# Kernel tuning notes

Measured on AMD Instinct MI355X. Metric: run time of the kernel, lower is better.

Reference implementation:

```python
import jax, jax.numpy as jnp
import numpy as np

N_NODES = 100000
N_EDGES = 1600000
D_IN = 128
LAYER_SIZES = [128, 128, 64]


def setup_inputs() -> dict:
    key = jax.random.key(0)
    ks = jax.random.split(key, 12)
    x = jax.random.normal(ks[0], (N_NODES, D_IN), dtype=jnp.float32)
    edge_index = jax.random.randint(ks[1], (2, N_EDGES), 0, N_NODES, dtype=jnp.int64)
    edge_weight = jax.random.uniform(ks[2], (N_EDGES,), dtype=jnp.float32)
    inp = {"x": x, "edge_index": edge_index, "edge_weight": edge_weight}
    dims = [D_IN] + LAYER_SIZES
    for i in range(len(LAYER_SIZES)):
        fan_in, fan_out = dims[i], dims[i + 1]
        # glorot-style init like PyG GCNConv
        scale = jnp.sqrt(6.0 / (fan_in + fan_out)).astype(jnp.float32)
        inp[f"W{i}"] = jax.random.uniform(ks[3 + 2 * i], (fan_in, fan_out), dtype=jnp.float32, minval=-scale, maxval=scale)
        inp[f"b{i}"] = jnp.zeros((fan_out,), dtype=jnp.float32)
    return inp


def _gcn_norm(edge_index, edge_weight, num_nodes):
    # PyG gcn_norm with add_self_loops=True (fill value 1.0)
    src, dst = edge_index[0], edge_index[1]
    loop = jnp.arange(num_nodes, dtype=edge_index.dtype)
    src_full = jnp.concatenate([src, loop])
    dst_full = jnp.concatenate([dst, loop])
    w_full = jnp.concatenate([edge_weight, jnp.ones((num_nodes,), dtype=edge_weight.dtype)])
    deg = jax.ops.segment_sum(w_full, dst_full, num_segments=num_nodes)  # [N]
    deg_inv_sqrt = jnp.where(deg > 0, jax.lax.rsqrt(jnp.where(deg > 0, deg, 1.0)), 0.0)
    norm = deg_inv_sqrt[src_full] * w_full * deg_inv_sqrt[dst_full]  # [E+N]
    return src_full, dst_full, norm


def _gcn_conv(x, src, dst, norm, W, b):
    h = x @ W                                  # [N, d_out] dense transform
    msg = h[src] * norm[:, None]               # [E+N, d_out] gather + scale
    out = jax.ops.segment_sum(msg, dst, num_segments=x.shape[0])  # scatter-add
    return out + b


def reference(x, edge_index, edge_weight, W0, b0, W1, b1, W2, b2):
    N = x.shape[0]
    src, dst, norm = _gcn_norm(edge_index, edge_weight, N)
    x = jax.nn.relu(_gcn_conv(x, src, dst, norm, W0, b0))
    x = jax.nn.relu(_gcn_conv(x, src, dst, norm, W1, b1))
    x = _gcn_conv(x, src, dst, norm, W2, b2)  # no ReLU on final layer
    return x
```

## Files before the change

kernel.cpp:

```cpp
#include <hip/hip_runtime.h>
#include <hip/hip_fp16.h>


typedef __attribute__((ext_vector_type(8))) _Float16 f16x8;
typedef __attribute__((ext_vector_type(4))) float f32x4;
typedef unsigned long long u64;

#define WQ_BITS 15
#define WQ_SCALE 32768.0f
#define WQ_MASK 32767u
#define MAXNP 2048

#define RL(v, k) __builtin_amdgcn_readlane((v), (k))

__global__ __launch_bounds__(256) void k_pre(int* tail, int NP,
                                             const float* __restrict__ W0,
                                             const float* __restrict__ W1,
                                             const float* __restrict__ W2,
                                             __half* __restrict__ wt0,
                                             __half* __restrict__ wt1,
                                             __half* __restrict__ wt2) {
    int id = blockIdx.x * 256 + threadIdx.x;
    if (id < NP) tail[id] = 0;
    if (id < 16384) {
        int n = id >> 7, k = id & 127;
        wt0[id] = __float2half(W0[k * 128 + n]);
    } else if (id < 32768) {
        int j = id - 16384, n = j >> 7, k = j & 127;
        wt1[j] = __float2half(W1[k * 128 + n]);
    } else if (id < 40960) {
        int j = id - 32768, n = j >> 7, k = j & 127;
        wt2[j] = __float2half(W2[k * 64 + n]);
    }
}

__global__ __launch_bounds__(256) void k_bin(const int* __restrict__ src,
                                             const int* __restrict__ dst,
                                             const float* __restrict__ w,
                                             int* tail, u64* __restrict__ glist,
                                             int E, int ecap, int NP, int shift) {
    __shared__ unsigned int h[MAXNP];
    __shared__ int base[MAXNP];
    const int nb = gridDim.x;
    const int per = (E + nb - 1) / nb;
    const int e0 = blockIdx.x * per;
    const int e1 = (e0 + per < E) ? e0 + per : E;

    for (int i = threadIdx.x; i < NP; i += 256) h[i] = 0;
    __syncthreads();
    for (int e = e0 + (int)threadIdx.x; e < e1; e += 256) {
        int p = dst[e] >> shift;
        atomicAdd(&h[p], 1u);
    }
    __syncthreads();
    for (int i = threadIdx.x; i < NP; i += 256) {
        unsigned int c = h[i];
        base[i] = c ? atomicAdd(&tail[i], (int)c) : 0;
    }
    __syncthreads();
    for (int e = e0 + (int)threadIdx.x; e < e1; e += 256) {
        int t = dst[e];
        int p = t >> shift;
        int s = __builtin_nontemporal_load(src + e);
        float we = __builtin_nontemporal_load(w + e);
        int wq = (int)(we * WQ_SCALE + 0.5f);
        wq = (wq < (int)WQ_MASK) ? wq : (int)WQ_MASK;
        u64 v = ((u64)(unsigned)t << 32) |
                ((unsigned)s << WQ_BITS) | (unsigned)wq;
        unsigned int idx = atomicSub(&h[p], 1u) - 1u;
        int pos = base[p] + (int)idx;
        if (pos < ecap) glist[(size_t)p * ecap + pos] = v;
    }
}

__global__ __launch_bounds__(256) void k_fill(const int* __restrict__ tail,
                                              const u64* __restrict__ glist,
                                              int ecap, int* __restrict__ cnt,
                                              float* __restrict__ dinv,
                                              unsigned int* __restrict__ EW,
                                              int cap, int N, int shift) {
    __shared__ unsigned int lcnt[MAXNP];
    __shared__ float lws[MAXNP];
    const int p = blockIdx.x;
    const int np = 1 << shift;
    const int t0 = p << shift;
    for (int i = threadIdx.x; i < np; i += 256) { lcnt[i] = 0; lws[i] = 0.f; }
    __syncthreads();
    int n = tail[p];
    if (n > ecap) n = ecap;
    const u64* L = glist + (size_t)p * ecap;
    for (int j = threadIdx.x; j < n; j += 256) {
        u64 v = L[j];
        int t = (int)(v >> 32);
        int loc = t - t0;
        unsigned int k = atomicAdd(&lcnt[loc], 1u);
        if ((int)k < cap) {
            EW[(size_t)t * cap + k] = (unsigned int)v;
            atomicAdd(&lws[loc], (float)((unsigned int)v & WQ_MASK));
        }
    }
    __syncthreads();
    for (int i = threadIdx.x; i < np; i += 256) {
        int t = t0 + i;
        if (t < N) {
            int c = (int)lcnt[i];
            c = (c < cap) ? c : cap;
            cnt[t] = c;
            dinv[t] = 1.0f / sqrtf(1.0f + lws[i] * (1.0f / WQ_SCALE));
        }
    }
}

template <int BN, bool XFP32>
__global__ __launch_bounds__(256, 4) void k_gemm(const void* __restrict__ Xv,
                                                 const __half* __restrict__ Wt,
                                                 const float* __restrict__ dinv,
                                                 __half* __restrict__ H, int N) {
    const int tid = threadIdx.x;
    const int lane = tid & 63;
    const int wv = tid >> 6;
    const int m = lane & 15;
    const int quad = lane >> 4;
    const int rb = blockIdx.x * 64;
    const int row = rb + wv * 16 + m;
    const int rowc = (row < N) ? row : (N - 1);

    f16x8 xf[4];
    if constexpr (XFP32) {
        const float* X = (const float*)Xv;
#pragma unroll
        for (int s = 0; s < 4; s++) {
            const float4* p = (const float4*)(X + (size_t)rowc * 128 + s * 32 + quad * 8);
            float4 u0 = p[0], u1 = p[1];
            f16x8 f;
            f[0] = (_Float16)u0.x; f[1] = (_Float16)u0.y;
            f[2] = (_Float16)u0.z; f[3] = (_Float16)u0.w;
            f[4] = (_Float16)u1.x; f[5] = (_Float16)u1.y;
            f[6] = (_Float16)u1.z; f[7] = (_Float16)u1.w;
            xf[s] = f;
        }
    } else {
        const __half* X = (const __half*)Xv;
#pragma unroll
        for (int s = 0; s < 4; s++)
            xf[s] = *(const f16x8*)(X + (size_t)rowc * 128 + s * 32 + quad * 8);
    }

    constexpr int NT = BN / 16;
    f32x4 acc[NT];
#pragma unroll
    for (int t = 0; t < NT; t++) acc[t] = (f32x4){0.f, 0.f, 0.f, 0.f};

#pragma unroll
    for (int s = 0; s < 4; s++) {
#pragma unroll
        for (int t = 0; t < NT; t++) {
            f16x8 wf = *(const f16x8*)(Wt + (size_t)(t * 16 + m) * 128 + s * 32 + quad * 8);
            acc[t] = __builtin_amdgcn_mfma_f32_16x16x32_f16(wf, xf[s], acc[t], 0, 0, 0);
        }
    }

    if (row < N) {
        float sc = dinv[row];
#pragma unroll
        for (int t = 0; t < NT; t++) {
            __half2 h0 = __floats2half2_rn(sc * acc[t][0], sc * acc[t][1]);
            __half2 h1 = __floats2half2_rn(sc * acc[t][2], sc * acc[t][3]);
            __half2* dstp = (__half2*)(H + (size_t)row * BN + t * 16 + quad * 4);
            dstp[0] = h0;
            dstp[1] = h1;
        }
    }
}

template <int DOUT, bool RELU>
__global__ __launch_bounds__(256) void k_agg(const __half* __restrict__ H,
                                             const unsigned int* __restrict__ EW,
                                             const int* __restrict__ cnt,
                                             const float* __restrict__ dinv,
                                             const float* __restrict__ bias,
                                             void* __restrict__ Outv,
                                             int N, int cap) {
    int node = blockIdx.x * 4 + (threadIdx.x >> 6);
    if (node >= N) return;
    const int lane = threadIdx.x & 63;

    int c = cnt[node];
    c = (c < cap) ? c : cap;

    unsigned int meta = 0;
    if (lane < c) meta = EW[(size_t)node * cap + lane];

    float dt = dinv[node];

    if constexpr (DOUT == 128) {
        const __half2* H2 = reinterpret_cast<const __half2*>(H);
        float2 hs = __half22float2(H2[(size_t)node * 64 + lane]);
        float a0 = hs.x, a1 = hs.y;
        int k = 0;
        for (; k + 8 <= c; k += 8) {
            __half2 hr[8]; float w[8];
#pragma unroll
            for (int u = 0; u < 8; u++) {
                unsigned int mm = RL(meta, k + u);
                w[u] = (float)(mm & WQ_MASK) * (1.0f / WQ_SCALE);
                hr[u] = H2[(size_t)(mm >> WQ_BITS) * 64 + lane];
            }
#pragma unroll
            for (int u = 0; u < 8; u++) {
                float2 hv = __half22float2(hr[u]);
                a0 = fmaf(w[u], hv.x, a0);
                a1 = fmaf(w[u], hv.y, a1);
            }
        }
        for (; k + 4 <= c; k += 4) {
            __half2 hr[4]; float w[4];
#pragma unroll
            for (int u = 0; u < 4; u++) {
                unsigned int mm = RL(meta, k + u);
                w[u] = (float)(mm & WQ_MASK) * (1.0f / WQ_SCALE);
                hr[u] = H2[(size_t)(mm >> WQ_BITS) * 64 + lane];
            }
#pragma unroll
            for (int u = 0; u < 4; u++) {
                float2 hv = __half22float2(hr[u]);
                a0 = fmaf(w[u], hv.x, a0);
                a1 = fmaf(w[u], hv.y, a1);
            }
        }
        for (; k < c; k++) {
            unsigned int mm = RL(meta, k);
            float w = (float)(mm & WQ_MASK) * (1.0f / WQ_SCALE);
            float2 hv = __half22float2(H2[(size_t)(mm >> WQ_BITS) * 64 + lane]);
            a0 = fmaf(w, hv.x, a0);
            a1 = fmaf(w, hv.y, a1);
        }
        float2 b = reinterpret_cast<const float2*>(bias)[lane];
        a0 = fmaf(dt, a0, b.x);
        a1 = fmaf(dt, a1, b.y);
        if (RELU) { a0 = fmaxf(a0, 0.f); a1 = fmaxf(a1, 0.f); }
        reinterpret_cast<__half2*>(Outv)[(size_t)node * 64 + lane] = __floats2half2_rn(a0, a1);
    } else {
        float a = __half2float(H[(size_t)node * 64 + lane]);
        int k = 0;
        for (; k + 8 <= c; k += 8) {
            __half hr[8]; float w[8];
#pragma unroll
            for (int u = 0; u < 8; u++) {
                unsigned int mm = RL(meta, k + u);
                w[u] = (float)(mm & WQ_MASK) * (1.0f / WQ_SCALE);
                hr[u] = H[(size_t)(mm >> WQ_BITS) * 64 + lane];
            }
#pragma unroll
            for (int u = 0; u < 8; u++) a = fmaf(w[u], __half2float(hr[u]), a);
        }
        for (; k < c; k++) {
            unsigned int mm = RL(meta, k);
            float w = (float)(mm & WQ_MASK) * (1.0f / WQ_SCALE);
            a = fmaf(w, __half2float(H[(size_t)(mm >> WQ_BITS) * 64 + lane]), a);
        }
        a = fmaf(dt, a, bias[lane]);
        if (RELU) a = fmaxf(a, 0.f);
        ((float*)Outv)[(size_t)node * 64 + lane] = a;
    }
}

extern "C" void kernel_launch(void* const* d_in, const int* in_sizes, int n_in,
                              void* d_out, int out_size, void* d_ws, size_t ws_size,
                              hipStream_t stream) {
    const int N = in_sizes[0] / 128;
    const int E = in_sizes[2];

    const float* x  = (const float*)d_in[0];
    const int*   ei = (const int*)d_in[1];
    const int*   src = ei;
    const int*   dst = ei + E;
    const float* ew  = (const float*)d_in[2];
    const float* W0 = (const float*)d_in[3];
    const float* b0 = (const float*)d_in[4];
    const float* W1 = (const float*)d_in[5];
    const float* b1 = (const float*)d_in[6];
    const float* W2 = (const float*)d_in[7];
    const float* b2 = (const float*)d_in[8];

    int shift = 6;
    while ((((N - 1) >> shift) + 1) > MAXNP) shift++;
    const int NP = ((N - 1) >> shift) + 1;

    size_t fixed = (((size_t)N * 4 + 255) & ~(size_t)255)
                 + (((size_t)N * 4 + 255) & ~(size_t)255)
                 + 2 * (((size_t)N * 128 * 2 + 255) & ~(size_t)255)
                 + 3 * 33024
                 + (((size_t)NP * 4 + 255) & ~(size_t)255)
                 + 2048;
    int cap = 64;
    if (ws_size > fixed) {
        size_t avail = (ws_size - fixed) / ((size_t)N * 4);
        if (avail < (size_t)cap) cap = (int)avail;
    } else {
        cap = 0;
    }

    char* p = (char*)d_ws;
    auto alloc = [&](size_t bytes) -> void* {
        void* r = (void*)p;
        p += (bytes + 255) & ~(size_t)255;
        return r;
    };
    int*          cnt  = (int*)alloc((size_t)N * 4);
    float*        dinv = (float*)alloc((size_t)N * 4);
    unsigned int* EW   = (unsigned int*)alloc((size_t)N * cap * 4);
    __half*       bufH = (__half*)alloc((size_t)N * 128 * 2);
    __half*       bufA = (__half*)alloc((size_t)N * 128 * 2);
    __half*       wt0  = (__half*)alloc(16384 * 2);
    __half*       wt1  = (__half*)alloc(16384 * 2);
    __half*       wt2  = (__half*)alloc(8192 * 2);
    int*          tail = (int*)alloc((size_t)NP * 4);

    u64* glist = (u64*)bufH;
    int  ecap  = (int)(((size_t)N * 128 * 2) / ((size_t)NP * 8));

    dim3 blk(256);
    int preN = (NP > 40960) ? NP : 40960;
    dim3 gPre((preN + 255) / 256);
    dim3 gBin(256);
    dim3 gFill(NP);
    dim3 gGemm((N + 63) / 64);
    dim3 gWave((N + 3) / 4);

    k_pre<<<gPre, blk, 0, stream>>>(tail, NP, W0, W1, W2, wt0, wt1, wt2);
    k_bin<<<gBin, blk, 0, stream>>>(src, dst, ew, tail, glist, E, ecap, NP, shift);
    k_fill<<<gFill, blk, 0, stream>>>(tail, glist, ecap, cnt, dinv, EW, cap, N, shift);

    k_gemm<128, true><<<gGemm, blk, 0, stream>>>(x, wt0, dinv, bufH, N);
    k_agg<128, true><<<gWave, blk, 0, stream>>>(bufH, EW, cnt, dinv, b0, bufA, N, cap);

    k_gemm<128, false><<<gGemm, blk, 0, stream>>>(bufA, wt1, dinv, bufH, N);
    k_agg<128, true><<<gWave, blk, 0, stream>>>(bufH, EW, cnt, dinv, b1, bufA, N, cap);

    k_gemm<64, false><<<gGemm, blk, 0, stream>>>(bufA, wt2, dinv, bufH, N);
    k_agg<64, false><<<gWave, blk, 0, stream>>>(bufH, EW, cnt, dinv, b2,
                                                d_out, N, cap);
}
```

Measured before the change: 435.7 us.

## Split 128-wide aggregation into two column-half passes

The 128-column aggregation kernel now covers only 32 half2 columns per launch, selected by a new column-offset argument, and is launched twice per layer (offsets 0 and 32). The likely aim is to halve the gathered feature working set per pass so that more of the randomly accessed rows stay in cache. In exchange, half of each wavefront's lanes sit idle, the edge metadata and readlane work are repeated, and the launch count doubles.

```diff
diff --git a/kernel.cpp b/kernel.cpp
--- a/kernel.cpp
+++ b/kernel.cpp
@@ -180,7 +180,7 @@
                                              const float* __restrict__ dinv,
                                              const float* __restrict__ bias,
                                              void* __restrict__ Outv,
-                                             int N, int cap) {
+                                             int N, int cap, int c0) {
     int node = blockIdx.x * 4 + (threadIdx.x >> 6);
     if (node >= N) return;
     const int lane = threadIdx.x & 63;
@@ -194,9 +194,14 @@
     float dt = dinv[node];
 
     if constexpr (DOUT == 128) {
+        const bool act = lane < 32;
+        const int col = c0 + (lane & 31);
         const __half2* H2 = reinterpret_cast<const __half2*>(H);
-        float2 hs = __half22float2(H2[(size_t)node * 64 + lane]);
-        float a0 = hs.x, a1 = hs.y;
+        float a0 = 0.f, a1 = 0.f;
+        if (act) {
+            float2 hs = __half22float2(H2[(size_t)node * 64 + col]);
+            a0 = hs.x; a1 = hs.y;
+        }
         int k = 0;
         for (; k + 8 <= c; k += 8) {
             __half2 hr[8]; float w[8];
@@ -204,13 +209,15 @@
             for (int u = 0; u < 8; u++) {
                 unsigned int mm = RL(meta, k + u);
                 w[u] = (float)(mm & WQ_MASK) * (1.0f / WQ_SCALE);
-                hr[u] = H2[(size_t)(mm >> WQ_BITS) * 64 + lane];
-            }
-#pragma unroll
-            for (int u = 0; u < 8; u++) {
-                float2 hv = __half22float2(hr[u]);
-                a0 = fmaf(w[u], hv.x, a0);
-                a1 = fmaf(w[u], hv.y, a1);
+                if (act) hr[u] = H2[(size_t)(mm >> WQ_BITS) * 64 + col];
+            }
+            if (act) {
+#pragma unroll
+                for (int u = 0; u < 8; u++) {
+                    float2 hv = __half22float2(hr[u]);
+                    a0 = fmaf(w[u], hv.x, a0);
+                    a1 = fmaf(w[u], hv.y, a1);
+                }
             }
         }
         for (; k + 4 <= c; k += 4) {
@@ -219,27 +226,33 @@
             for (int u = 0; u < 4; u++) {
                 unsigned int mm = RL(meta, k + u);
                 w[u] = (float)(mm & WQ_MASK) * (1.0f / WQ_SCALE);
-                hr[u] = H2[(size_t)(mm >> WQ_BITS) * 64 + lane];
-            }
-#pragma unroll
-            for (int u = 0; u < 4; u++) {
-                float2 hv = __half22float2(hr[u]);
-                a0 = fmaf(w[u], hv.x, a0);
-                a1 = fmaf(w[u], hv.y, a1);
+                if (act) hr[u] = H2[(size_t)(mm >> WQ_BITS) * 64 + col];
+            }
+            if (act) {
+#pragma unroll
+                for (int u = 0; u < 4; u++) {
+                    float2 hv = __half22float2(hr[u]);
+                    a0 = fmaf(w[u], hv.x, a0);
+                    a1 = fmaf(w[u], hv.y, a1);
+                }
             }
         }
         for (; k < c; k++) {
             unsigned int mm = RL(meta, k);
             float w = (float)(mm & WQ_MASK) * (1.0f / WQ_SCALE);
-            float2 hv = __half22float2(H2[(size_t)(mm >> WQ_BITS) * 64 + lane]);
-            a0 = fmaf(w, hv.x, a0);
-            a1 = fmaf(w, hv.y, a1);
-        }
-        float2 b = reinterpret_cast<const float2*>(bias)[lane];
-        a0 = fmaf(dt, a0, b.x);
-        a1 = fmaf(dt, a1, b.y);
-        if (RELU) { a0 = fmaxf(a0, 0.f); a1 = fmaxf(a1, 0.f); }
-        reinterpret_cast<__half2*>(Outv)[(size_t)node * 64 + lane] = __floats2half2_rn(a0, a1);
+            if (act) {
+                float2 hv = __half22float2(H2[(size_t)(mm >> WQ_BITS) * 64 + col]);
+                a0 = fmaf(w, hv.x, a0);
+                a1 = fmaf(w, hv.y, a1);
+            }
+        }
+        if (act) {
+            float2 b = reinterpret_cast<const float2*>(bias)[col];
+            a0 = fmaf(dt, a0, b.x);
+            a1 = fmaf(dt, a1, b.y);
+            if (RELU) { a0 = fmaxf(a0, 0.f); a1 = fmaxf(a1, 0.f); }
+            reinterpret_cast<__half2*>(Outv)[(size_t)node * 64 + col] = __floats2half2_rn(a0, a1);
+        }
     } else {
         float a = __half2float(H[(size_t)node * 64 + lane]);
         int k = 0;
@@ -333,12 +346,14 @@
     k_fill<<<gFill, blk, 0, stream>>>(tail, glist, ecap, cnt, dinv, EW, cap, N, shift);
 
     k_gemm<128, true><<<gGemm, blk, 0, stream>>>(x, wt0, dinv, bufH, N);
-    k_agg<128, true><<<gWave, blk, 0, stream>>>(bufH, EW, cnt, dinv, b0, bufA, N, cap);
+    k_agg<128, true><<<gWave, blk, 0, stream>>>(bufH, EW, cnt, dinv, b0, bufA, N, cap, 0);
+    k_agg<128, true><<<gWave, blk, 0, stream>>>(bufH, EW, cnt, dinv, b0, bufA, N, cap, 32);
 
     k_gemm<128, false><<<gGemm, blk, 0, stream>>>(bufA, wt1, dinv, bufH, N);
-    k_agg<128, true><<<gWave, blk, 0, stream>>>(bufH, EW, cnt, dinv, b1, bufA, N, cap);
+    k_agg<128, true><<<gWave, blk, 0, stream>>>(bufH, EW, cnt, dinv, b1, bufA, N, cap, 0);
+    k_agg<128, true><<<gWave, blk, 0, stream>>>(bufH, EW, cnt, dinv, b1, bufA, N, cap, 32);
 
     k_gemm<64, false><<<gGemm, blk, 0, stream>>>(bufA, wt2, dinv, bufH, N);
     k_agg<64, false><<<gWave, blk, 0, stream>>>(bufH, EW, cnt, dinv, b2,
-                                                d_out, N, cap);
-}
+                                                d_out, N, cap, 0);
+}
```

New measurement: 552.6 us. 26.8% more time.

## Split wavefront across neighbors with 16-byte row loads and shuffle reduction

Applied to the files above, without the earlier changes.

The aggregation kernel now assigns sub-groups of lanes to different neighbors, with each lane loading 8 fp16 features as one 16-byte vector, instead of having the whole wavefront read one neighbor's row two features per lane. Partial sums are combined with xor shuffles and only the first sub-group writes the output. This is meant to raise memory-level parallelism and use wider loads for the gather-heavy SpMM. In exchange it adds cross-lane reductions, uses __shfl instead of readlane to fetch per-lane edge metadata, and leaves idle lanes in the tail loop when a node has few neighbors.

```diff
diff --git a/kernel.cpp b/kernel.cpp
--- a/kernel.cpp
+++ b/kernel.cpp
@@ -11,7 +11,7 @@
 #define WQ_MASK 32767u
 #define MAXNP 2048
 
-#define RL(v, k) __builtin_amdgcn_readlane((v), (k))
+#define SHFLU(v, k) ((unsigned int)__shfl((int)(v), (k), 64))
 
 __global__ __launch_bounds__(256) void k_pre(int* tail, int NP,
                                              const float* __restrict__ W0,
@@ -194,74 +194,112 @@
     float dt = dinv[node];
 
     if constexpr (DOUT == 128) {
-        const __half2* H2 = reinterpret_cast<const __half2*>(H);
-        float2 hs = __half22float2(H2[(size_t)node * 64 + lane]);
-        float a0 = hs.x, a1 = hs.y;
+        const int part = lane & 15;
+        const int q = lane >> 4;
+        float acc[8];
+#pragma unroll
+        for (int j = 0; j < 8; j++) acc[j] = 0.f;
+
         int k = 0;
-        for (; k + 8 <= c; k += 8) {
-            __half2 hr[8]; float w[8];
-#pragma unroll
-            for (int u = 0; u < 8; u++) {
-                unsigned int mm = RL(meta, k + u);
-                w[u] = (float)(mm & WQ_MASK) * (1.0f / WQ_SCALE);
-                hr[u] = H2[(size_t)(mm >> WQ_BITS) * 64 + lane];
+        for (; k + 16 <= c; k += 16) {
+            f16x8 hv[4];
+            float w[4];
+#pragma unroll
+            for (int g = 0; g < 4; g++) {
+                unsigned int mm = SHFLU(meta, k + g * 4 + q);
+                w[g] = (float)(mm & WQ_MASK) * (1.0f / WQ_SCALE);
+                hv[g] = *(const f16x8*)(H + (size_t)(mm >> WQ_BITS) * 128 + part * 8);
             }
 #pragma unroll
-            for (int u = 0; u < 8; u++) {
-                float2 hv = __half22float2(hr[u]);
-                a0 = fmaf(w[u], hv.x, a0);
-                a1 = fmaf(w[u], hv.y, a1);
+            for (int g = 0; g < 4; g++)
+#pragma unroll
+                for (int j = 0; j < 8; j++)
+                    acc[j] = fmaf(w[g], (float)hv[g][j], acc[j]);
+        }
+        for (; k < c; k += 4) {
+            int idx = k + q;
+            unsigned int mm = SHFLU(meta, (idx < c) ? idx : 0);
+            float w = (idx < c) ? (float)(mm & WQ_MASK) * (1.0f / WQ_SCALE) : 0.f;
+            unsigned int row = (idx < c) ? (mm >> WQ_BITS) : (unsigned int)node;
+            f16x8 hv = *(const f16x8*)(H + (size_t)row * 128 + part * 8);
+#pragma unroll
+            for (int j = 0; j < 8; j++)
+                acc[j] = fmaf(w, (float)hv[j], acc[j]);
+        }
+#pragma unroll
+        for (int j = 0; j < 8; j++) {
+            acc[j] += __shfl_xor(acc[j], 16, 64);
+            acc[j] += __shfl_xor(acc[j], 32, 64);
+        }
+        if (q == 0) {
+            f16x8 sv = *(const f16x8*)(H + (size_t)node * 128 + part * 8);
+            f32x4 b0v = *(const f32x4*)(bias + part * 8);
+            f32x4 b1v = *(const f32x4*)(bias + part * 8 + 4);
+            f16x8 ov;
+#pragma unroll
+            for (int j = 0; j < 8; j++) {
+                float bj = (j < 4) ? b0v[j] : b1v[j - 4];
+                float v = fmaf(dt, acc[j] + (float)sv[j], bj);
+                if (RELU) v = fmaxf(v, 0.f);
+                ov[j] = (_Float16)v;
             }
-        }
-        for (; k + 4 <= c; k += 4) {
-            __half2 hr[4]; float w[4];
-#pragma unroll
-            for (int u = 0; u < 4; u++) {
-                unsigned int mm = RL(meta, k + u);
-                w[u] = (float)(mm & WQ_MASK) * (1.0f / WQ_SCALE);
-                hr[u] = H2[(size_t)(mm >> WQ_BITS) * 64 + lane];
+            *(f16x8*)((__half*)Outv + (size_t)node * 128 + part * 8) = ov;
+        }
+    } else {
+        const int part = lane & 7;
+        const int q = lane >> 3;
+        float acc[8];
+#pragma unroll
+        for (int j = 0; j < 8; j++) acc[j] = 0.f;
+
+        int k = 0;
+        for (; k + 32 <= c; k += 32) {
+            f16x8 hv[4];
+            float w[4];
+#pragma unroll
+            for (int g = 0; g < 4; g++) {
+                unsigned int mm = SHFLU(meta, k + g * 8 + q);
+                w[g] = (float)(mm & WQ_MASK) * (1.0f / WQ_SCALE);
+                hv[g] = *(const f16x8*)(H + (size_t)(mm >> WQ_BITS) * 64 + part * 8);
             }
 #pragma unroll
-            for (int u = 0; u < 4; u++) {
-                float2 hv = __half22float2(hr[u]);
-                a0 = fmaf(w[u], hv.x, a0);
-                a1 = fmaf(w[u], hv.y, a1);
+            for (int g = 0; g < 4; g++)
+#pragma unroll
+                for (int j = 0; j < 8; j++)
+                    acc[j] = fmaf(w[g], (float)hv[g][j], acc[j]);
+        }
+        for (; k < c; k += 8) {
+            int idx = k + q;
+            unsigned int mm = SHFLU(meta, (idx < c) ? idx : 0);
+            float w = (idx < c) ? (float)(mm & WQ_MASK) * (1.0f / WQ_SCALE) : 0.f;
+            unsigned int row = (idx < c) ? (mm >> WQ_BITS) : (unsigned int)node;
+            f16x8 hv = *(const f16x8*)(H + (size_t)row * 64 + part * 8);
+#pragma unroll
+            for (int j = 0; j < 8; j++)
+                acc[j] = fmaf(w, (float)hv[j], acc[j]);
+        }
+#pragma unroll
+        for (int j = 0; j < 8; j++) {
+            acc[j] += __shfl_xor(acc[j], 8, 64);
+            acc[j] += __shfl_xor(acc[j], 16, 64);
+            acc[j] += __shfl_xor(acc[j], 32, 64);
+        }
+        if (q == 0) {
+            f16x8 sv = *(const f16x8*)(H + (size_t)node * 64 + part * 8);
+            f32x4 b0v = *(const f32x4*)(bias + part * 8);
+            f32x4 b1v = *(const f32x4*)(bias + part * 8 + 4);
+            f32x4 o0, o1;
+#pragma unroll
+            for (int j = 0; j < 8; j++) {
+                float bj = (j < 4) ? b0v[j] : b1v[j - 4];
+                float v = fmaf(dt, acc[j] + (float)sv[j], bj);
+                if (RELU) v = fmaxf(v, 0.f);
+                if (j < 4) o0[j] = v; else o1[j - 4] = v;
             }
-        }
-        for (; k < c; k++) {
-            unsigned int mm = RL(meta, k);
-            float w = (float)(mm & WQ_MASK) * (1.0f / WQ_SCALE);
-            float2 hv = __half22float2(H2[(size_t)(mm >> WQ_BITS) * 64 + lane]);
-            a0 = fmaf(w, hv.x, a0);
-            a1 = fmaf(w, hv.y, a1);
-        }
-        float2 b = reinterpret_cast<const float2*>(bias)[lane];
-        a0 = fmaf(dt, a0, b.x);
-        a1 = fmaf(dt, a1, b.y);
-        if (RELU) { a0 = fmaxf(a0, 0.f); a1 = fmaxf(a1, 0.f); }
-        reinterpret_cast<__half2*>(Outv)[(size_t)node * 64 + lane] = __floats2half2_rn(a0, a1);
-    } else {
-        float a = __half2float(H[(size_t)node * 64 + lane]);
-        int k = 0;
-        for (; k + 8 <= c; k += 8) {
-            __half hr[8]; float w[8];
-#pragma unroll
-            for (int u = 0; u < 8; u++) {
-                unsigned int mm = RL(meta, k + u);
-                w[u] = (float)(mm & WQ_MASK) * (1.0f / WQ_SCALE);
-                hr[u] = H[(size_t)(mm >> WQ_BITS) * 64 + lane];
-            }
-#pragma unroll
-            for (int u = 0; u < 8; u++) a = fmaf(w[u], __half2float(hr[u]), a);
-        }
-        for (; k < c; k++) {
-            unsigned int mm = RL(meta, k);
-            float w = (float)(mm & WQ_MASK) * (1.0f / WQ_SCALE);
-            a = fmaf(w, __half2float(H[(size_t)(mm >> WQ_BITS) * 64 + lane]), a);
-        }
-        a = fmaf(dt, a, bias[lane]);
-        if (RELU) a = fmaxf(a, 0.f);
-        ((float*)Outv)[(size_t)node * 64 + lane] = a;
+            float* op = (float*)Outv + (size_t)node * 64 + part * 8;
+            *(f32x4*)op = o0;
+            *(f32x4*)(op + 4) = o1;
+        }
     }
 }
 
```

New measurement: 427.3 us. Within noise of the previous version (-1.9%).
